# Kernel optimization log

Measured on AMD Instinct MI355X. Metric: run time of the kernel, lower is better.

## Reference

```python
import jax, jax.numpy as jnp
import numpy as np

N_EMBD = 768
N_HEAD = 12
HEAD_DIM = N_EMBD // N_HEAD
B = 4
L_MAIN = 1024
L_SIDE = 1024
HALF = L_SIDE // 2  # occurrences of each modality per row
LN_EPS = 1e-5


def setup_inputs() -> dict:
    key = jax.random.key(0)
    ks = jax.random.split(key, 16)
    x = jax.random.normal(ks[0], (B, L_MAIN, N_EMBD), jnp.float32)
    # ages in years, sorted per-row (events arrive in time order), all >= 0
    age = jnp.sort(jax.random.uniform(ks[1], (B, L_MAIN), jnp.float32) * 80.0, axis=1)
    mod_age = jnp.sort(jax.random.uniform(ks[2], (B, L_SIDE), jnp.float32) * 80.0, axis=1)
    # each row holds exactly HALF tokens of modality 2 and HALF of modality 3, randomly interleaved
    base = jnp.concatenate([jnp.full((HALF,), 2, jnp.int32), jnp.full((HALF,), 3, jnp.int32)])
    mod_idx = jax.vmap(lambda k: jax.random.permutation(k, base))(jax.random.split(ks[3], B))
    mod2_emb = jax.random.normal(ks[4], (B * HALF, N_EMBD), jnp.float32)
    mod3_emb = jax.random.normal(ks[5], (B * HALF, N_EMBD), jnp.float32)

    def lin(k, fan_out, fan_in):
        return 0.02 * jax.random.normal(k, (fan_out, fan_in), jnp.float32)

    params = dict(
        ln0_w=jnp.ones((N_EMBD,), jnp.float32), ln0_b=jnp.zeros((N_EMBD,), jnp.float32),
        ln1_w=jnp.ones((N_EMBD,), jnp.float32), ln1_b=jnp.zeros((N_EMBD,), jnp.float32),
        ln2_w=jnp.ones((N_EMBD,), jnp.float32), ln2_b=jnp.zeros((N_EMBD,), jnp.float32),
        q_w=lin(ks[6], N_EMBD, N_EMBD), q_b=jnp.zeros((N_EMBD,), jnp.float32),
        k_w=lin(ks[7], N_EMBD, N_EMBD), k_b=jnp.zeros((N_EMBD,), jnp.float32),
        v_w=lin(ks[8], N_EMBD, N_EMBD), v_b=jnp.zeros((N_EMBD,), jnp.float32),
        c_w=lin(ks[9], N_EMBD, N_EMBD), c_b=jnp.zeros((N_EMBD,), jnp.float32),
        fc_w=lin(ks[10], 4 * N_EMBD, N_EMBD), fc_b=jnp.zeros((4 * N_EMBD,), jnp.float32),
        proj_w=lin(ks[11], N_EMBD, 4 * N_EMBD), proj_b=jnp.zeros((N_EMBD,), jnp.float32),
    )
    return dict(x=x, age=age, mod_idx=mod_idx, mod_age=mod_age,
                mod2_emb=mod2_emb, mod3_emb=mod3_emb, **params)


def _ln(t, w, b):
    m = jnp.mean(t, axis=-1, keepdims=True)
    v = jnp.var(t, axis=-1, keepdims=True)
    return (t - m) * jax.lax.rsqrt(v + LN_EPS) * w + b


def _fuse_embed(mod_idx, mod_age, mod2_emb, mod3_emb):
    # torch: stable argsort by age, then scatter each modality's embeddings into
    # its matching positions in row-major nonzero order.
    order = jnp.argsort(mod_age, axis=1, stable=True)
    s_idx = jnp.take_along_axis(mod_idx, order, axis=1)  # [B, L_side]
    rows = jnp.arange(s_idx.shape[0])[:, None]
    def scatter_mod(val, m_emb):
        mask = s_idx == val
        occ = jnp.cumsum(mask, axis=1) - 1          # per-row occurrence counter
        gidx = rows * HALF + jnp.clip(occ, 0, HALF - 1)  # global row-major index
        return jnp.where(mask[..., None], m_emb[gidx], 0.0)
    return scatter_mod(2, mod2_emb) + scatter_mod(3, mod3_emb)


def _cross_fusion(x, age, mod_idx, mod_age, mod2_emb, mod3_emb,
                  ln0_w, ln0_b, ln1_w, ln1_b, ln2_w, ln2_b,
                  q_w, q_b, k_w, k_b, v_w, v_b, c_w, c_b,
                  fc_w, fc_b, proj_w, proj_b):
    mod_x = _fuse_embed(mod_idx, mod_age, mod2_emb, mod3_emb)  # [B, L_side, E]
    # time_attention_mask: query may attend to keys with key_age <= query_age, pad = key_age >= 0
    attn_mask = (age[:, :, None] >= mod_age[:, None, :]) & (mod_age >= 0.0)[:, None, :]
    attn_mask = attn_mask[:, None, :, :]  # [B, 1, L_main, L_side]

    xn = _ln(x, ln1_w, ln1_b)
    sn = _ln(mod_x, ln0_w, ln0_b)
    q = (xn @ q_w.T + q_b).reshape(B, L_MAIN, N_HEAD, HEAD_DIM).transpose(0, 2, 1, 3)
    k = (sn @ k_w.T + k_b).reshape(B, L_SIDE, N_HEAD, HEAD_DIM).transpose(0, 2, 1, 3)
    v = (sn @ v_w.T + v_b).reshape(B, L_SIDE, N_HEAD, HEAD_DIM).transpose(0, 2, 1, 3)

    att = jnp.einsum('bhqd,bhkd->bhqk', q, k) * (HEAD_DIM ** -0.5)
    all_masked = ~jnp.any(attn_mask, axis=-1, keepdims=True)
    # fully-masked rows: use 0 logits (uniform softmax) then zero out -> matches
    # torch's masked_fill(all_masked, 0) after nan softmax, but grad-safe.
    neg = jnp.where(all_masked, 0.0, -jnp.inf)
    att = jnp.where(attn_mask, att, neg)
    att = jax.nn.softmax(att, axis=-1)
    att = jnp.where(all_masked, 0.0, att)

    y = jnp.einsum('bhqk,bhkd->bhqd', att, v)
    y = y.transpose(0, 2, 1, 3).reshape(B, L_MAIN, N_EMBD)
    x = x + (y @ c_w.T + c_b)
    h = _ln(x, ln2_w, ln2_b)
    h = jax.nn.gelu(h @ fc_w.T + fc_b, approximate=False)
    x = x + (h @ proj_w.T + proj_b)
    return x


def reference(x, age, mod_idx, mod_age, mod2_emb, mod3_emb,
              ln0_w, ln0_b, ln1_w, ln1_b, ln2_w, ln2_b,
              q_w, q_b, k_w, k_b, v_w, v_b, c_w, c_b,
              fc_w, fc_b, proj_w, proj_b):
    return _cross_fusion(x, age, mod_idx, mod_age, mod2_emb, mod3_emb,
                         ln0_w, ln0_b, ln1_w, ln1_b, ln2_w, ln2_b,
                         q_w, q_b, k_w, k_b, v_w, v_b, c_w, c_b,
                         fc_w, fc_b, proj_w, proj_b)
```

## Files before the change

kernel.cpp:

```cpp
#include <hip/hip_runtime.h>

#define N_EMBD 768
#define SEQ    1024
#define NBATCH 4
#define NHEAD  12
#define HDIM   64
#define NROWS  4096
#define FFN    3072
#define W768   589824
#define WFC    2359296
#define NCVT   6912

typedef unsigned short u16;
typedef __bf16 bf16x8 __attribute__((ext_vector_type(8)));
typedef float  f32x4  __attribute__((ext_vector_type(4)));
typedef unsigned short u16x8 __attribute__((ext_vector_type(8)));

typedef const __attribute__((address_space(1))) unsigned int gu32;
typedef __attribute__((address_space(3))) unsigned int lu32;
#define GLL(g, l) __builtin_amdgcn_global_load_lds((gu32*)(g), (lu32*)(l), 16, 0, 0)

__device__ __forceinline__ u16 f2bf(float f) {
    union { float f; unsigned int i; } v; v.f = f;
    unsigned int r = v.i + 0x7fffu + ((v.i >> 16) & 1u);
    return (u16)(r >> 16);
}

__global__ __launch_bounds__(256) void prep_kernel(const float* __restrict__ qw,
                                                   const float* __restrict__ kw,
                                                   const float* __restrict__ vw,
                                                   const float* __restrict__ cw,
                                                   const float* __restrict__ fcw,
                                                   const float* __restrict__ pw,
                                                   u16* __restrict__ wdst,
                                                   const float* __restrict__ x,
                                                   const float* __restrict__ ln1w,
                                                   const float* __restrict__ ln1b,
                                                   u16* __restrict__ xn,
                                                   const int* __restrict__ mod_idx,
                                                   int* __restrict__ g) {
    int bx = blockIdx.x;
    if (bx < NCVT) {
        size_t e = ((size_t)bx * 256 + threadIdx.x) * 4;
        const float* src; size_t base;
        if      (e < 1 * (size_t)W768) { src = qw;  base = 0; }
        else if (e < 2 * (size_t)W768) { src = kw;  base = 1 * (size_t)W768; }
        else if (e < 3 * (size_t)W768) { src = vw;  base = 2 * (size_t)W768; }
        else if (e < 4 * (size_t)W768) { src = cw;  base = 3 * (size_t)W768; }
        else if (e < 4 * (size_t)W768 + WFC) { src = fcw; base = 4 * (size_t)W768; }
        else { src = pw; base = 4 * (size_t)W768 + WFC; }
        float4 v = *(const float4*)(src + (e - base));
        ushort4 o;
        o.x = f2bf(v.x); o.y = f2bf(v.y); o.z = f2bf(v.z); o.w = f2bf(v.w);
        *(ushort4*)(wdst + e) = o;
    } else if (bx < NCVT + 1024) {
        int row  = (bx - NCVT) * 4 + (threadIdx.x >> 6);
        int lane = threadIdx.x & 63;
        const float* p = x + (size_t)row * N_EMBD;
        float vals[12];
        float s = 0.f, sq = 0.f;
#pragma unroll
        for (int c = 0; c < 12; c++) {
            float v = p[c * 64 + lane];
            vals[c] = v; s += v; sq += v * v;
        }
#pragma unroll
        for (int o = 32; o > 0; o >>= 1) { s += __shfl_xor(s, o); sq += __shfl_xor(sq, o); }
        float mean = s * (1.0f / 768.0f);
        float var  = sq * (1.0f / 768.0f) - mean * mean;
        float r    = rsqrtf(var + 1e-5f);
        u16* d = xn + (size_t)row * N_EMBD;
#pragma unroll
        for (int c = 0; c < 12; c++) {
            int idx = c * 64 + lane;
            d[idx] = f2bf((vals[c] - mean) * r * ln1w[idx] + ln1b[idx]);
        }
    } else {
        __shared__ int sc[256];
        int b = bx - NCVT - 1024;
        int j = threadIdx.x;
        int4 mi = *(const int4*)(mod_idx + b * SEQ + j * 4);
        int f0 = (mi.x == 2), f1 = (mi.y == 2), f2v = (mi.z == 2), f3 = (mi.w == 2);
        int t1 = f0 + f1, t2 = t1 + f2v, t3 = t2 + f3;
        sc[j] = t3;
        __syncthreads();
        for (int off = 1; off < 256; off <<= 1) {
            int add = (j >= off) ? sc[j - off] : 0;
            __syncthreads();
            sc[j] += add;
            __syncthreads();
        }
        int excl = sc[j] - t3;
        int cin[4] = {excl + f0, excl + t1, excl + t2, excl + t3};
        int fl[4] = {f0, f1, f2v, f3};
#pragma unroll
        for (int i2 = 0; i2 < 4; i2++) {
            int jj = j * 4 + i2;
            int occ = fl[i2] ? (cin[i2] - 1) : (jj - cin[i2]);
            occ = occ < 0 ? 0 : (occ > 511 ? 511 : occ);
            g[b * SEQ + jj] = fl[i2] ? (b * 512 + occ) : (2048 + b * 512 + occ);
        }
    }
}

__global__ __launch_bounds__(256) void ln_rows(const float* __restrict__ src,
                                               const float* __restrict__ src2,
                                               const int* __restrict__ g,
                                               const float* __restrict__ w,
                                               const float* __restrict__ b,
                                               u16* __restrict__ dst) {
    int row  = blockIdx.x * 4 + (threadIdx.x >> 6);
    int lane = threadIdx.x & 63;
    const float* p;
    if (g) {
        int gi = g[row];
        p = (gi < 2048) ? (src + (size_t)gi * N_EMBD)
                        : (src2 + (size_t)(gi - 2048) * N_EMBD);
    } else {
        p = src + (size_t)row * N_EMBD;
    }
    float vals[12];
    float s = 0.f, sq = 0.f;
#pragma unroll
    for (int c = 0; c < 12; c++) {
        float v = p[c * 64 + lane];
        vals[c] = v; s += v; sq += v * v;
    }
#pragma unroll
    for (int o = 32; o > 0; o >>= 1) { s += __shfl_xor(s, o); sq += __shfl_xor(sq, o); }
    float mean = s * (1.0f / 768.0f);
    float var  = sq * (1.0f / 768.0f) - mean * mean;
    float r    = rsqrtf(var + 1e-5f);
    u16* d = dst + (size_t)row * N_EMBD;
#pragma unroll
    for (int c = 0; c < 12; c++) {
        int idx = c * 64 + lane;
        d[idx] = f2bf((vals[c] - mean) * r * w[idx] + b[idx]);
    }
}

__device__ __forceinline__ void core128(const u16* __restrict__ A, const u16* __restrict__ W,
                                        int K, int m0, int n0, int t,
                                        u16* As, u16* Bs, f32x4 (&acc)[4][4]) {
    int w = t >> 6, lane = t & 63, quad = lane >> 4, l16 = lane & 15;
    int r16 = lane >> 2, c8 = (lane & 3) * 8;
    int wm = (w >> 1) * 64, wn = (w & 1) * 64;
    for (int k0 = 0; k0 < K; k0 += 32) {
        __syncthreads();
        const u16* ga = A + (size_t)(m0 + w * 32 + r16) * K + k0 + c8;
        const u16* gb = W + (size_t)(n0 + w * 32 + r16) * K + k0 + c8;
        GLL(ga,                  &As[(w * 32) * 32]);
        GLL(ga + 16 * (size_t)K, &As[(w * 32 + 16) * 32]);
        GLL(gb,                  &Bs[(w * 32) * 32]);
        GLL(gb + 16 * (size_t)K, &Bs[(w * 32 + 16) * 32]);
        __syncthreads();
        bf16x8 af[4], bfr[4];
#pragma unroll
        for (int i = 0; i < 4; i++)
            af[i] = *(const bf16x8*)&As[(wm + i * 16 + l16) * 32 + quad * 8];
#pragma unroll
        for (int j = 0; j < 4; j++)
            bfr[j] = *(const bf16x8*)&Bs[(wn + j * 16 + l16) * 32 + quad * 8];
#pragma unroll
        for (int i = 0; i < 4; i++)
#pragma unroll
            for (int j = 0; j < 4; j++)
                acc[i][j] = __builtin_amdgcn_mfma_f32_16x16x32_bf16(af[i], bfr[j], acc[i][j], 0, 0, 0);
    }
}

__device__ __forceinline__ void core64(const u16* __restrict__ A, const u16* __restrict__ W,
                                       int K, int kBeg, int kEnd, int m0, int n0, int t,
                                       u16* As, u16* Bs, f32x4 (&acc)[2][4]) {
    int w = t >> 6, lane = t & 63, quad = lane >> 4, l16 = lane & 15;
    int r16 = lane >> 2, c8 = (lane & 3) * 8;
    int wm = (w >> 1) * 32, wn = (w & 1) * 64;
    for (int k0 = kBeg; k0 < kEnd; k0 += 32) {
        __syncthreads();
        const u16* gb = W + (size_t)(n0 + w * 32 + r16) * K + k0 + c8;
        GLL(A + (size_t)(m0 + w * 16 + r16) * K + k0 + c8, &As[(w * 16) * 32]);
        GLL(gb,                  &Bs[(w * 32) * 32]);
        GLL(gb + 16 * (size_t)K, &Bs[(w * 32 + 16) * 32]);
        __syncthreads();
        bf16x8 af[2], bfr[4];
#pragma unroll
        for (int i = 0; i < 2; i++)
            af[i] = *(const bf16x8*)&As[(wm + i * 16 + l16) * 32 + quad * 8];
#pragma unroll
        for (int j = 0; j < 4; j++)
            bfr[j] = *(const bf16x8*)&Bs[(wn + j * 16 + l16) * 32 + quad * 8];
#pragma unroll
        for (int i = 0; i < 2; i++)
#pragma unroll
            for (int j = 0; j < 4; j++)
                acc[i][j] = __builtin_amdgcn_mfma_f32_16x16x32_bf16(af[i], bfr[j], acc[i][j], 0, 0, 0);
    }
}

__global__ __launch_bounds__(256) void gemm_qkv(const u16* __restrict__ xn,
                                                const u16* __restrict__ sn,
                                                const u16* __restrict__ wq,
                                                const float* __restrict__ qb,
                                                const float* __restrict__ kb,
                                                const float* __restrict__ vb,
                                                u16* __restrict__ outbase) {
    __shared__ u16 As[128 * 32], Bs[128 * 32];
    int bxg = blockIdx.x;
    int c = bxg & 7, s = bxg >> 3;
    int mg = s / 18, r = s % 18;
    int z = r / 6, n = r % 6;
    int m0 = (mg * 8 + c) * 128, n0 = n * 128;
    const u16* A = (z == 0) ? xn : sn;
    const u16* W = wq + (size_t)z * W768;
    const float* bias = (z == 0) ? qb : ((z == 1) ? kb : vb);
    u16* C = outbase + (size_t)z * ((size_t)NROWS * N_EMBD);
    int t = threadIdx.x;
    f32x4 acc[4][4];
#pragma unroll
    for (int i = 0; i < 4; i++)
#pragma unroll
        for (int j = 0; j < 4; j++) acc[i][j] = (f32x4){0.f, 0.f, 0.f, 0.f};
    core128(A, W, N_EMBD, m0, n0, t, As, Bs, acc);
    int w = t >> 6, lane = t & 63, quad = lane >> 4, l16 = lane & 15;
    int wm = (w >> 1) * 64, wn = (w & 1) * 64;
#pragma unroll
    for (int j = 0; j < 4; j++) {
        int col = n0 + wn + j * 16 + l16;
        float bv = bias[col];
#pragma unroll
        for (int i = 0; i < 4; i++) {
            int rowb = m0 + wm + i * 16 + quad * 4;
#pragma unroll
            for (int r2 = 0; r2 < 4; r2++)
                C[(size_t)(rowb + r2) * N_EMBD + col] = f2bf(acc[i][j][r2] + bv);
        }
    }
}

__global__ __launch_bounds__(256) void gemm_fc(const u16* __restrict__ A,
                                               const u16* __restrict__ W,
                                               const float* __restrict__ bias,
                                               u16* __restrict__ C) {
    __shared__ u16 As[128 * 32], Bs[128 * 32];
    int bxg = blockIdx.x;
    int c = bxg & 7, s = bxg >> 3;
    int mg = s / 24, n = s % 24;
    int m0 = (mg * 8 + c) * 128, n0 = n * 128;
    int t = threadIdx.x;
    f32x4 acc[4][4];
#pragma unroll
    for (int i = 0; i < 4; i++)
#pragma unroll
        for (int j = 0; j < 4; j++) acc[i][j] = (f32x4){0.f, 0.f, 0.f, 0.f};
    core128(A, W, N_EMBD, m0, n0, t, As, Bs, acc);
    int w = t >> 6, lane = t & 63, quad = lane >> 4, l16 = lane & 15;
    int wm = (w >> 1) * 64, wn = (w & 1) * 64;
#pragma unroll
    for (int j = 0; j < 4; j++) {
        int col = n0 + wn + j * 16 + l16;
        float bv = bias[col];
#pragma unroll
        for (int i = 0; i < 4; i++) {
            int rowb = m0 + wm + i * 16 + quad * 4;
#pragma unroll
            for (int r = 0; r < 4; r++) {
                float v = acc[i][j][r] + bv;
                float y = v * (1.595769122f + 0.071354816f * v * v);
                float gel = v / (1.0f + __expf(-y));
                C[(size_t)(rowb + r) * FFN + col] = f2bf(gel);
            }
        }
    }
}

__global__ __launch_bounds__(256) void gemm_cproj(const u16* __restrict__ A,
                                                  const u16* __restrict__ W,
                                                  const float* __restrict__ bias,
                                                  const float* __restrict__ Res,
                                                  float* __restrict__ C) {
    __shared__ u16 As[64 * 32], Bs[128 * 32];
    int m0 = blockIdx.y * 64, n0 = blockIdx.x * 128;
    int t = threadIdx.x;
    f32x4 acc[2][4];
#pragma unroll
    for (int i = 0; i < 2; i++)
#pragma unroll
        for (int j = 0; j < 4; j++) acc[i][j] = (f32x4){0.f, 0.f, 0.f, 0.f};
    core64(A, W, N_EMBD, 0, N_EMBD, m0, n0, t, As, Bs, acc);
    int w = t >> 6, lane = t & 63, quad = lane >> 4, l16 = lane & 15;
    int wm = (w >> 1) * 32, wn = (w & 1) * 64;
#pragma unroll
    for (int j = 0; j < 4; j++) {
        int col = n0 + wn + j * 16 + l16;
        float bv = bias[col];
#pragma unroll
        for (int i = 0; i < 2; i++) {
            int rowb = m0 + wm + i * 16 + quad * 4;
#pragma unroll
            for (int r = 0; r < 4; r++) {
                size_t idx = (size_t)(rowb + r) * N_EMBD + col;
                C[idx] = acc[i][j][r] + bv + Res[idx];
            }
        }
    }
}

__global__ __launch_bounds__(256) void gemm_proj_split(const u16* __restrict__ A,
                                                       const u16* __restrict__ W,
                                                       float* __restrict__ p0,
                                                       float* __restrict__ p1) {
    __shared__ u16 As[64 * 32], Bs[128 * 32];
    int bxg = blockIdx.x;
    int c = bxg & 7, s = bxg >> 3;
    int mg = s / 12, r = s % 12;
    int z = r / 6, n = r % 6;
    int m0 = (mg * 8 + c) * 64, n0 = n * 128;
    float* P = z ? p1 : p0;
    int t = threadIdx.x;
    f32x4 acc[2][4];
#pragma unroll
    for (int i = 0; i < 2; i++)
#pragma unroll
        for (int j = 0; j < 4; j++) acc[i][j] = (f32x4){0.f, 0.f, 0.f, 0.f};
    core64(A, W, FFN, z * (FFN / 2), (z + 1) * (FFN / 2), m0, n0, t, As, Bs, acc);
    int w = t >> 6, lane = t & 63, quad = lane >> 4, l16 = lane & 15;
    int wm = (w >> 1) * 32, wn = (w & 1) * 64;
#pragma unroll
    for (int j = 0; j < 4; j++) {
        int col = n0 + wn + j * 16 + l16;
#pragma unroll
        for (int i = 0; i < 2; i++) {
            int rowb = m0 + wm + i * 16 + quad * 4;
#pragma unroll
            for (int r2 = 0; r2 < 4; r2++)
                P[(size_t)(rowb + r2) * N_EMBD + col] = acc[i][j][r2];
        }
    }
}

__global__ __launch_bounds__(256) void reduce_proj(const float* __restrict__ p0,
                                                   const float* __restrict__ p1,
                                                   const float* __restrict__ bias,
                                                   const float* __restrict__ x1,
                                                   float* __restrict__ out) {
    size_t idx = ((size_t)blockIdx.x * 256 + threadIdx.x) * 4;
    int col = (int)(idx % N_EMBD);
    float4 a = *(const float4*)(p0 + idx);
    float4 b = *(const float4*)(p1 + idx);
    float4 r = *(const float4*)(x1 + idx);
    float4 bb = *(const float4*)(bias + col);
    float4 o;
    o.x = a.x + b.x + r.x + bb.x;
    o.y = a.y + b.y + r.y + bb.y;
    o.z = a.z + b.z + r.z + bb.z;
    o.w = a.w + b.w + r.w + bb.w;
    *(float4*)(out + idx) = o;
}

#define KST 72

__global__ __launch_bounds__(256) void attn_kernel(const u16* __restrict__ Q,
                                                   const u16* __restrict__ K,
                                                   const u16* __restrict__ V,
                                                   const float* __restrict__ age,
                                                   const float* __restrict__ mod_age,
                                                   u16* __restrict__ Y) {
    __shared__ u16 Kl[64 * KST];
    __shared__ u16 Vt[64 * KST];
    __shared__ u16 Pl[4][16 * KST];

    int bx = blockIdx.x;
    int qt = 15 - (bx / 48);
    int bh = bx % 48;
    int b = bh / NHEAD, h = bh % NHEAD;
    int t = threadIdx.x;
    int w = t >> 6, lane = t & 63, quad = lane >> 4, l16 = lane & 15;
    int q0 = qt * 64 + w * 16;

    size_t qrowbase = ((size_t)(b * SEQ + q0 + l16)) * N_EMBD + h * HDIM;
    bf16x8 qf0 = *(const bf16x8*)&Q[qrowbase + quad * 8];
    bf16x8 qf1 = *(const bf16x8*)&Q[qrowbase + 32 + quad * 8];

    float age_r[4];
#pragma unroll
    for (int r = 0; r < 4; r++) age_r[r] = age[b * SEQ + q0 + quad * 4 + r];
    float age_q0      = __shfl(age_r[0], 0);
    float age_max_blk = age[b * SEQ + qt * 64 + 63];
    float mod_min     = mod_age[b * SEQ];

    float mv0 = (lane < 16) ? mod_age[b * SEQ + lane * 64] : 1e30f;
    unsigned long long bm = __ballot(mv0 > age_max_blk);
    int nkt = bm ? (__ffsll(bm) - 1) : 16;

    int krow0 = t >> 3,        kc8 = (t & 7) * 8;
    int krow1 = 32 + (t >> 3);
    int vrow  = t & 63;
    int vc8_0 = t >> 6, vc8_1 = 4 + (t >> 6);

    float m_i[4] = {-1e30f, -1e30f, -1e30f, -1e30f};
    float l_i[4] = {0.f, 0.f, 0.f, 0.f};
    f32x4 o[4];
#pragma unroll
    for (int nt = 0; nt < 4; nt++) o[nt] = (f32x4){0.f, 0.f, 0.f, 0.f};

    u16x8 kr0, kr1, vr0, vr1;
    float mreg = 0.f;
    if (nkt > 0) {
        size_t kb = ((size_t)(b * SEQ)) * N_EMBD + h * HDIM;
        kr0 = *(const u16x8*)(K + kb + (size_t)krow0 * N_EMBD + kc8);
        kr1 = *(const u16x8*)(K + kb + (size_t)krow1 * N_EMBD + kc8);
        vr0 = *(const u16x8*)(V + kb + (size_t)vrow * N_EMBD + vc8_0 * 8);
        vr1 = *(const u16x8*)(V + kb + (size_t)vrow * N_EMBD + vc8_1 * 8);
        mreg = mod_age[b * SEQ + lane];
    }

    for (int kt = 0; kt < nkt; kt++) {
        __syncthreads();
        *(u16x8*)&Kl[krow0 * KST + kc8] = kr0;
        *(u16x8*)&Kl[krow1 * KST + kc8] = kr1;
#pragma unroll
        for (int e = 0; e < 8; e++) Vt[(vc8_0 * 8 + e) * KST + vrow] = vr0[e];
#pragma unroll
        for (int e = 0; e < 8; e++) Vt[(vc8_1 * 8 + e) * KST + vrow] = vr1[e];
        float mcur = mreg;
        __syncthreads();

        if (kt + 1 < nkt) {
            size_t kb = ((size_t)(b * SEQ + (kt + 1) * 64)) * N_EMBD + h * HDIM;
            kr0 = *(const u16x8*)(K + kb + (size_t)krow0 * N_EMBD + kc8);
            kr1 = *(const u16x8*)(K + kb + (size_t)krow1 * N_EMBD + kc8);
            vr0 = *(const u16x8*)(V + kb + (size_t)vrow * N_EMBD + vc8_0 * 8);
            vr1 = *(const u16x8*)(V + kb + (size_t)vrow * N_EMBD + vc8_1 * 8);
            mreg = mod_age[b * SEQ + (kt + 1) * 64 + lane];
        }

        float tile_max = __shfl(mcur, 63);
        bool need_mask = tile_max > age_q0;
        float p[4][4];
#pragma unroll
        for (int jt = 0; jt < 4; jt++) {
            f32x4 s = (f32x4){0.f, 0.f, 0.f, 0.f};
            bf16x8 kf0 = *(const bf16x8*)&Kl[(jt * 16 + l16) * KST + quad * 8];
            bf16x8 kf1 = *(const bf16x8*)&Kl[(jt * 16 + l16) * KST + 32 + quad * 8];
            s = __builtin_amdgcn_mfma_f32_16x16x32_bf16(qf0, kf0, s, 0, 0, 0);
            s = __builtin_amdgcn_mfma_f32_16x16x32_bf16(qf1, kf1, s, 0, 0, 0);
            float mval = __shfl(mcur, jt * 16 + l16);
#pragma unroll
            for (int r = 0; r < 4; r++) {
                float sv = s[r] * 0.125f;
                p[jt][r] = (!need_mask || mval <= age_r[r]) ? sv : -1e30f;
            }
        }
        float alpha[4];
#pragma unroll
        for (int r = 0; r < 4; r++) {
            float mx = fmaxf(fmaxf(p[0][r], p[1][r]), fmaxf(p[2][r], p[3][r]));
#pragma unroll
            for (int msk = 1; msk < 16; msk <<= 1) mx = fmaxf(mx, __shfl_xor(mx, msk));
            float mnew = fmaxf(m_i[r], mx);
            alpha[r] = __expf(m_i[r] - mnew);
            float srow = 0.f;
#pragma unroll
            for (int jt = 0; jt < 4; jt++) {
                float pv = __expf(p[jt][r] - mnew);
                p[jt][r] = pv;
                srow += pv;
            }
#pragma unroll
            for (int msk = 1; msk < 16; msk <<= 1) srow += __shfl_xor(srow, msk);
            l_i[r] = l_i[r] * alpha[r] + srow;
            m_i[r] = mnew;
        }
#pragma unroll
        for (int jt = 0; jt < 4; jt++)
#pragma unroll
            for (int r = 0; r < 4; r++)
                Pl[w][(quad * 4 + r) * KST + jt * 16 + l16] = f2bf(p[jt][r]);
#pragma unroll
        for (int nt = 0; nt < 4; nt++)
#pragma unroll
            for (int r = 0; r < 4; r++) o[nt][r] *= alpha[r];
#pragma unroll
        for (int c = 0; c < 2; c++) {
            bf16x8 pf = *(const bf16x8*)&Pl[w][l16 * KST + c * 32 + quad * 8];
#pragma unroll
            for (int nt = 0; nt < 4; nt++) {
                bf16x8 vf = *(const bf16x8*)&Vt[(nt * 16 + l16) * KST + c * 32 + quad * 8];
                o[nt] = __builtin_amdgcn_mfma_f32_16x16x32_bf16(pf, vf, o[nt], 0, 0, 0);
            }
        }
    }
#pragma unroll
    for (int r = 0; r < 4; r++) {
        int qrow = q0 + quad * 4 + r;
        float inv = (age_r[r] >= mod_min) ? (1.0f / l_i[r]) : 0.0f;
#pragma unroll
        for (int nt = 0; nt < 4; nt++)
            Y[((size_t)(b * SEQ + qrow)) * N_EMBD + h * HDIM + nt * 16 + l16] =
                f2bf(o[nt][r] * inv);
    }
}

extern "C" void kernel_launch(void* const* d_in, const int* in_sizes, int n_in,
                              void* d_out, int out_size, void* d_ws, size_t ws_size,
                              hipStream_t stream) {
    const float* x       = (const float*)d_in[0];
    const float* age     = (const float*)d_in[1];
    const int*   mod_idx = (const int*)d_in[2];
    const float* mod_age = (const float*)d_in[3];
    const float* mod2    = (const float*)d_in[4];
    const float* mod3    = (const float*)d_in[5];
    const float* ln0w = (const float*)d_in[6],  *ln0b = (const float*)d_in[7];
    const float* ln1w = (const float*)d_in[8],  *ln1b = (const float*)d_in[9];
    const float* ln2w = (const float*)d_in[10], *ln2b = (const float*)d_in[11];
    const float* qb = (const float*)d_in[13];
    const float* kb = (const float*)d_in[15];
    const float* vb = (const float*)d_in[17];
    const float* cb = (const float*)d_in[19];
    const float* fcb = (const float*)d_in[21];
    const float* pb = (const float*)d_in[23];

    char* ws = (char*)d_ws;
    const size_t RB = (size_t)NROWS * N_EMBD * 2;
    int* g   = (int*)ws;
    u16* wq  = (u16*)(ws + 32768);
    u16* wc  = wq + 3 * (size_t)W768;
    u16* wfc = wq + 4 * (size_t)W768;
    u16* wp  = wq + 4 * (size_t)W768 + WFC;
    size_t off = 32768 + 2 * (4 * (size_t)W768 + 2 * (size_t)WFC);
    u16* xn   = (u16*)(ws + off); off += RB;
    u16* sn   = (u16*)(ws + off); off += RB;
    u16* qbuf = (u16*)(ws + off); off += RB;
    u16* kbuf = (u16*)(ws + off); off += RB;
    u16* vbuf = (u16*)(ws + off); off += RB;
    float* x1 = (float*)(ws + off); off += (size_t)NROWS * N_EMBD * 4;
    u16* hbuf = (u16*)(ws + off);
    u16* yb = xn;  u16* hn = qbuf;
    float* p0 = (float*)xn;
    float* p1 = (float*)kbuf;

    prep_kernel<<<NCVT + 1024 + NBATCH, 256, 0, stream>>>(
        (const float*)d_in[12], (const float*)d_in[14], (const float*)d_in[16],
        (const float*)d_in[18], (const float*)d_in[20], (const float*)d_in[22], wq,
        x, ln1w, ln1b, xn, mod_idx, g);
    ln_rows<<<NROWS / 4, 256, 0, stream>>>(mod2, mod3, g, ln0w, ln0b, sn);

    gemm_qkv<<<576, 256, 0, stream>>>(xn, sn, wq, qb, kb, vb, qbuf);

    attn_kernel<<<NBATCH * NHEAD * 16, 256, 0, stream>>>(qbuf, kbuf, vbuf, age, mod_age, yb);

    gemm_cproj<<<dim3(N_EMBD / 128, NROWS / 64), 256, 0, stream>>>(yb, wc, cb, x, x1);
    ln_rows<<<NROWS / 4, 256, 0, stream>>>(x1, nullptr, nullptr, ln2w, ln2b, hn);
    gemm_fc<<<768, 256, 0, stream>>>(hn, wfc, fcb, hbuf);
    gemm_proj_split<<<768, 256, 0, stream>>>(hbuf, wp, p0, p1);
    reduce_proj<<<(NROWS * N_EMBD / 4) / 256, 256, 0, stream>>>(p0, p1, pb, x1, (float*)d_out);

    (void)in_sizes; (void)n_in; (void)out_size; (void)ws_size;
}
```

Before: 299.4 us.

## Process 128-key tiles per attention iteration and swizzle c_proj blocks by XCD

The attention kernel now stages two 64-key K/V tiles at once, 128 keys per loop iteration. This halves the number of barrier-separated iterations and doubles the MFMA work between barriers, using larger LDS buffers and more registers. For odd tile counts the extra 64-key tile is fully masked, because its keys are all later than every query in the block. Separately, gemm_cproj moves to a 1D grid remapped so that blocks landing on the same XCD share A-row tiles across all N columns, to improve L2 reuse.

```diff
diff --git a/kernel.cpp b/kernel.cpp
--- a/kernel.cpp
+++ b/kernel.cpp
@@ -279,7 +279,10 @@
                                                   const float* __restrict__ Res,
                                                   float* __restrict__ C) {
     __shared__ u16 As[64 * 32], Bs[128 * 32];
-    int m0 = blockIdx.y * 64, n0 = blockIdx.x * 128;
+    int bxg = blockIdx.x;
+    int c = bxg & 7, s = bxg >> 3;
+    int mg = s / 6, n = s % 6;
+    int m0 = (mg * 8 + c) * 64, n0 = n * 128;
     int t = threadIdx.x;
     f32x4 acc[2][4];
 #pragma unroll
@@ -357,7 +360,8 @@
     *(float4*)(out + idx) = o;
 }
 
-#define KST 72
+#define KST2 72
+#define VST2 136
 
 __global__ __launch_bounds__(256) void attn_kernel(const u16* __restrict__ Q,
                                                    const u16* __restrict__ K,
@@ -365,9 +369,9 @@
                                                    const float* __restrict__ age,
                                                    const float* __restrict__ mod_age,
                                                    u16* __restrict__ Y) {
-    __shared__ u16 Kl[64 * KST];
-    __shared__ u16 Vt[64 * KST];
-    __shared__ u16 Pl[4][16 * KST];
+    __shared__ u16 Kl[128 * KST2];
+    __shared__ u16 Vt[64 * VST2];
+    __shared__ u16 Pl[4][16 * VST2];
 
     int bx = blockIdx.x;
     int qt = 15 - (bx / 48);
@@ -391,11 +395,10 @@
     float mv0 = (lane < 16) ? mod_age[b * SEQ + lane * 64] : 1e30f;
     unsigned long long bm = __ballot(mv0 > age_max_blk);
     int nkt = bm ? (__ffsll(bm) - 1) : 16;
-
-    int krow0 = t >> 3,        kc8 = (t & 7) * 8;
-    int krow1 = 32 + (t >> 3);
-    int vrow  = t & 63;
-    int vc8_0 = t >> 6, vc8_1 = 4 + (t >> 6);
+    int nit = (nkt + 1) >> 1;
+
+    int krow_b = t >> 3, kc8 = (t & 7) * 8;
+    int vrow   = t & 63, vcb = t >> 6;
 
     float m_i[4] = {-1e30f, -1e30f, -1e30f, -1e30f};
     float l_i[4] = {0.f, 0.f, 0.f, 0.f};
@@ -403,48 +406,61 @@
 #pragma unroll
     for (int nt = 0; nt < 4; nt++) o[nt] = (f32x4){0.f, 0.f, 0.f, 0.f};
 
-    u16x8 kr0, kr1, vr0, vr1;
-    float mreg = 0.f;
-    if (nkt > 0) {
+    u16x8 kr[4], vr[4];
+    float mreg0 = 0.f, mreg1 = 0.f;
+    if (nit > 0) {
         size_t kb = ((size_t)(b * SEQ)) * N_EMBD + h * HDIM;
-        kr0 = *(const u16x8*)(K + kb + (size_t)krow0 * N_EMBD + kc8);
-        kr1 = *(const u16x8*)(K + kb + (size_t)krow1 * N_EMBD + kc8);
-        vr0 = *(const u16x8*)(V + kb + (size_t)vrow * N_EMBD + vc8_0 * 8);
-        vr1 = *(const u16x8*)(V + kb + (size_t)vrow * N_EMBD + vc8_1 * 8);
-        mreg = mod_age[b * SEQ + lane];
-    }
-
-    for (int kt = 0; kt < nkt; kt++) {
-        __syncthreads();
-        *(u16x8*)&Kl[krow0 * KST + kc8] = kr0;
-        *(u16x8*)&Kl[krow1 * KST + kc8] = kr1;
-#pragma unroll
-        for (int e = 0; e < 8; e++) Vt[(vc8_0 * 8 + e) * KST + vrow] = vr0[e];
-#pragma unroll
-        for (int e = 0; e < 8; e++) Vt[(vc8_1 * 8 + e) * KST + vrow] = vr1[e];
-        float mcur = mreg;
-        __syncthreads();
-
-        if (kt + 1 < nkt) {
-            size_t kb = ((size_t)(b * SEQ + (kt + 1) * 64)) * N_EMBD + h * HDIM;
-            kr0 = *(const u16x8*)(K + kb + (size_t)krow0 * N_EMBD + kc8);
-            kr1 = *(const u16x8*)(K + kb + (size_t)krow1 * N_EMBD + kc8);
-            vr0 = *(const u16x8*)(V + kb + (size_t)vrow * N_EMBD + vc8_0 * 8);
-            vr1 = *(const u16x8*)(V + kb + (size_t)vrow * N_EMBD + vc8_1 * 8);
-            mreg = mod_age[b * SEQ + (kt + 1) * 64 + lane];
-        }
-
-        float tile_max = __shfl(mcur, 63);
+#pragma unroll
+        for (int i = 0; i < 4; i++)
+            kr[i] = *(const u16x8*)(K + kb + (size_t)(i * 32 + krow_b) * N_EMBD + kc8);
+        vr[0] = *(const u16x8*)(V + kb + (size_t)vrow * N_EMBD + vcb * 8);
+        vr[1] = *(const u16x8*)(V + kb + (size_t)vrow * N_EMBD + (vcb + 4) * 8);
+        vr[2] = *(const u16x8*)(V + kb + (size_t)(64 + vrow) * N_EMBD + vcb * 8);
+        vr[3] = *(const u16x8*)(V + kb + (size_t)(64 + vrow) * N_EMBD + (vcb + 4) * 8);
+        mreg0 = mod_age[b * SEQ + lane];
+        mreg1 = mod_age[b * SEQ + 64 + lane];
+    }
+
+    for (int it = 0; it < nit; it++) {
+        __syncthreads();
+#pragma unroll
+        for (int i = 0; i < 4; i++)
+            *(u16x8*)&Kl[(i * 32 + krow_b) * KST2 + kc8] = kr[i];
+#pragma unroll
+        for (int e = 0; e < 8; e++) {
+            Vt[(vcb * 8 + e) * VST2 + vrow]            = vr[0][e];
+            Vt[((vcb + 4) * 8 + e) * VST2 + vrow]      = vr[1][e];
+            Vt[(vcb * 8 + e) * VST2 + 64 + vrow]       = vr[2][e];
+            Vt[((vcb + 4) * 8 + e) * VST2 + 64 + vrow] = vr[3][e];
+        }
+        float mc0 = mreg0, mc1 = mreg1;
+        __syncthreads();
+
+        if (it + 1 < nit) {
+            size_t kb = ((size_t)(b * SEQ + (it + 1) * 128)) * N_EMBD + h * HDIM;
+#pragma unroll
+            for (int i = 0; i < 4; i++)
+                kr[i] = *(const u16x8*)(K + kb + (size_t)(i * 32 + krow_b) * N_EMBD + kc8);
+            vr[0] = *(const u16x8*)(V + kb + (size_t)vrow * N_EMBD + vcb * 8);
+            vr[1] = *(const u16x8*)(V + kb + (size_t)vrow * N_EMBD + (vcb + 4) * 8);
+            vr[2] = *(const u16x8*)(V + kb + (size_t)(64 + vrow) * N_EMBD + vcb * 8);
+            vr[3] = *(const u16x8*)(V + kb + (size_t)(64 + vrow) * N_EMBD + (vcb + 4) * 8);
+            mreg0 = mod_age[b * SEQ + (it + 1) * 128 + lane];
+            mreg1 = mod_age[b * SEQ + (it + 1) * 128 + 64 + lane];
+        }
+
+        float tile_max = __shfl(mc1, 63);
         bool need_mask = tile_max > age_q0;
-        float p[4][4];
-#pragma unroll
-        for (int jt = 0; jt < 4; jt++) {
+        float p[8][4];
+#pragma unroll
+        for (int jt = 0; jt < 8; jt++) {
             f32x4 s = (f32x4){0.f, 0.f, 0.f, 0.f};
-            bf16x8 kf0 = *(const bf16x8*)&Kl[(jt * 16 + l16) * KST + quad * 8];
-            bf16x8 kf1 = *(const bf16x8*)&Kl[(jt * 16 + l16) * KST + 32 + quad * 8];
+            bf16x8 kf0 = *(const bf16x8*)&Kl[(jt * 16 + l16) * KST2 + quad * 8];
+            bf16x8 kf1 = *(const bf16x8*)&Kl[(jt * 16 + l16) * KST2 + 32 + quad * 8];
             s = __builtin_amdgcn_mfma_f32_16x16x32_bf16(qf0, kf0, s, 0, 0, 0);
             s = __builtin_amdgcn_mfma_f32_16x16x32_bf16(qf1, kf1, s, 0, 0, 0);
-            float mval = __shfl(mcur, jt * 16 + l16);
+            float mval = (jt < 4) ? __shfl(mc0, jt * 16 + l16)
+                                  : __shfl(mc1, (jt - 4) * 16 + l16);
 #pragma unroll
             for (int r = 0; r < 4; r++) {
                 float sv = s[r] * 0.125f;
@@ -454,14 +470,16 @@
         float alpha[4];
 #pragma unroll
         for (int r = 0; r < 4; r++) {
-            float mx = fmaxf(fmaxf(p[0][r], p[1][r]), fmaxf(p[2][r], p[3][r]));
+            float mx = p[0][r];
+#pragma unroll
+            for (int jt = 1; jt < 8; jt++) mx = fmaxf(mx, p[jt][r]);
 #pragma unroll
             for (int msk = 1; msk < 16; msk <<= 1) mx = fmaxf(mx, __shfl_xor(mx, msk));
             float mnew = fmaxf(m_i[r], mx);
             alpha[r] = __expf(m_i[r] - mnew);
             float srow = 0.f;
 #pragma unroll
-            for (int jt = 0; jt < 4; jt++) {
+            for (int jt = 0; jt < 8; jt++) {
                 float pv = __expf(p[jt][r] - mnew);
                 p[jt][r] = pv;
                 srow += pv;
@@ -472,20 +490,20 @@
             m_i[r] = mnew;
         }
 #pragma unroll
-        for (int jt = 0; jt < 4; jt++)
+        for (int jt = 0; jt < 8; jt++)
 #pragma unroll
             for (int r = 0; r < 4; r++)
-                Pl[w][(quad * 4 + r) * KST + jt * 16 + l16] = f2bf(p[jt][r]);
+                Pl[w][(quad * 4 + r) * VST2 + jt * 16 + l16] = f2bf(p[jt][r]);
 #pragma unroll
         for (int nt = 0; nt < 4; nt++)
 #pragma unroll
             for (int r = 0; r < 4; r++) o[nt][r] *= alpha[r];
 #pragma unroll
-        for (int c = 0; c < 2; c++) {
-            bf16x8 pf = *(const bf16x8*)&Pl[w][l16 * KST + c * 32 + quad * 8];
+        for (int c = 0; c < 4; c++) {
+            bf16x8 pf = *(const bf16x8*)&Pl[w][l16 * VST2 + c * 32 + quad * 8];
 #pragma unroll
             for (int nt = 0; nt < 4; nt++) {
-                bf16x8 vf = *(const bf16x8*)&Vt[(nt * 16 + l16) * KST + c * 32 + quad * 8];
+                bf16x8 vf = *(const bf16x8*)&Vt[(nt * 16 + l16) * VST2 + c * 32 + quad * 8];
                 o[nt] = __builtin_amdgcn_mfma_f32_16x16x32_bf16(pf, vf, o[nt], 0, 0, 0);
             }
         }
@@ -549,7 +567,7 @@
 
     attn_kernel<<<NBATCH * NHEAD * 16, 256, 0, stream>>>(qbuf, kbuf, vbuf, age, mod_age, yb);
 
-    gemm_cproj<<<dim3(N_EMBD / 128, NROWS / 64), 256, 0, stream>>>(yb, wc, cb, x, x1);
+    gemm_cproj<<<384, 256, 0, stream>>>(yb, wc, cb, x, x1);
     ln_rows<<<NROWS / 4, 256, 0, stream>>>(x1, nullptr, nullptr, ln2w, ln2b, hn);
     gemm_fc<<<768, 256, 0, stream>>>(hn, wfc, fcb, hbuf);
     gemm_proj_split<<<768, 256, 0, stream>>>(hbuf, wp, p0, p1);
```

Measured after the change: 293.5 us. 2.0% less time.
